# Performance work log

Hardware: AMD Instinct MI355X
Metric: run time of the kernel (lower is better)

Reference implementation:

```python
import jax, jax.numpy as jnp
import numpy as np

N = 4096
IN_F = 512
OUT_F = 256
HEADS = 4
HEAD_DIM = OUT_F // HEADS


def setup_inputs() -> dict:
    key = jax.random.key(0)
    k_feat, k_adj, k_w, k_a = jax.random.split(key, 4)
    features = jax.random.normal(k_feat, (N, IN_F), dtype=jnp.float32)
    adj_matrix = jax.random.uniform(k_adj, (N, N), dtype=jnp.float32)
    # xavier-uniform-ish init scaled small
    W = jax.random.normal(k_w, (OUT_F, IN_F), dtype=jnp.float32) * (1.0 / np.sqrt(IN_F))
    a = jax.random.normal(k_a, (HEADS, 2 * HEAD_DIM), dtype=jnp.float32) * 0.1
    bias = jnp.zeros((OUT_F,), dtype=jnp.float32)
    return {"features": features, "adj_matrix": adj_matrix, "W": W, "a": a, "bias": bias}


def reference(features, adj_matrix, W, a, bias):
    n = features.shape[0]
    h = features @ W.T                      # [N, OUT_F]
    hh = h.reshape(n, HEADS, HEAD_DIM)      # [N, H, D]
    # e[i,j,h] = leaky_relu(<h_i, a[:, :D]> + <h_j, a[:, D:]>) -- additive decomposition
    e_src = jnp.einsum('nhd,hd->nh', hh, a[:, :HEAD_DIM])   # [N, H]
    e_dst = jnp.einsum('nhd,hd->nh', hh, a[:, HEAD_DIM:])   # [N, H]
    e = e_src[:, None, :] + e_dst[None, :, :]               # [N, N, H]
    e = jnp.where(e >= 0, e, 0.2 * e)                       # leaky_relu(0.2)
    mask = adj_matrix[:, :, None] > 0.1                     # [N, N, 1]
    e = jnp.where(mask, e, -jnp.inf)
    attention = jax.nn.softmax(e, axis=1)                   # softmax over j
    attention = jnp.nan_to_num(attention, nan=0.0)          # fully-masked rows -> 0
    attention_mean = attention.mean(axis=2)                 # [N, N]
    h_out = attention_mean @ h + bias                       # [N, OUT_F]
    return h_out
```

## Files before the change

### kernel.cpp

```cpp
#include <hip/hip_runtime.h>
#include <math.h>

#define NN      4096
#define INF_    512
#define OUTF    256
#define NHEAD   4
#define HDIM    64
#define KSPLIT  8

typedef __attribute__((ext_vector_type(8))) short  short8x;
typedef __attribute__((ext_vector_type(4))) float  float4x;
typedef __attribute__((ext_vector_type(2))) float  float2x;

__device__ __forceinline__ unsigned short f2bf(float x) {
    union { float f; unsigned int u; } c; c.f = x;
    unsigned int r = (c.u + 0x7FFFu + ((c.u >> 16) & 1u)) >> 16;
    return (unsigned short)r;
}
__device__ __forceinline__ unsigned int cvtpk_bf16(float lo, float hi) {
    unsigned int r;
    asm("v_cvt_pk_bf16_f32 %0, %1, %2" : "=v"(r) : "v"(lo), "v"(hi));
    return r;
}
__device__ __forceinline__ float2x bf2up(unsigned int u) {
    union { unsigned int x; float f; } lo, hi;
    lo.x = u << 16; hi.x = u & 0xFFFF0000u;
    float2x r; r[0] = lo.f; r[1] = hi.f; return r;
}
__device__ __forceinline__ float2x max2(float2x a, float2x b) {
    float2x r; r[0] = fmaxf(a[0], b[0]); r[1] = fmaxf(a[1], b[1]); return r;
}

__global__ __launch_bounds__(256) void k_hedge(const float* __restrict__ feat,
                                               const float* __restrict__ W,
                                               const float* __restrict__ a,
                                               const float* __restrict__ bias,
                                               unsigned short* __restrict__ hT,
                                               float* __restrict__ es,
                                               unsigned short* __restrict__ Bt,
                                               unsigned short* __restrict__ Dt,
                                               float* __restrict__ out) {
    __shared__ __align__(16) unsigned short lds_f[16 * 72];
    __shared__ __align__(16) unsigned short lds_w[256 * 72];
    const int tid  = threadIdx.x;
    const int w    = tid >> 6;
    const int lane = tid & 63;
    const int lidx = lane & 15;
    const int quad = lane >> 4;
    const int i0   = blockIdx.x * 16;

    {
        float4x bv = *(const float4x*)(bias + ((tid * 4) & 255));
        float* ob = out + (size_t)i0 * OUTF;
        #pragma unroll
        for (int itr = 0; itr < 4; ++itr)
            *(float4x*)(ob + itr * 1024 + tid * 4) = bv;
    }

    const int fr = tid >> 4;
    const int fc = (tid & 15) * 4;
    const int wr = tid >> 2;
    const int wc = (tid & 3) * 16;

    float4x acc[4];
    #pragma unroll
    for (int q = 0; q < 4; ++q)
        acc[q] = (float4x){0.f, 0.f, 0.f, 0.f};

    for (int kt = 0; kt < INF_; kt += 64) {
        __syncthreads();
        {
            float4x v = *(const float4x*)&feat[(size_t)(i0 + fr) * INF_ + kt + fc];
            uint2 u;
            u.x = cvtpk_bf16(v[0], v[1]);
            u.y = cvtpk_bf16(v[2], v[3]);
            *(uint2*)&lds_f[fr * 72 + fc] = u;
        }
        #pragma unroll
        for (int p = 0; p < 4; ++p) {
            int row = p * 64 + wr;
            const float* src = &W[(size_t)row * INF_ + kt + wc];
            float4x v0 = *(const float4x*)(src);
            float4x v1 = *(const float4x*)(src + 4);
            float4x v2 = *(const float4x*)(src + 8);
            float4x v3 = *(const float4x*)(src + 12);
            union { short8x s; unsigned int u[4]; } p0, p1;
            p0.u[0] = cvtpk_bf16(v0[0], v0[1]); p0.u[1] = cvtpk_bf16(v0[2], v0[3]);
            p0.u[2] = cvtpk_bf16(v1[0], v1[1]); p0.u[3] = cvtpk_bf16(v1[2], v1[3]);
            p1.u[0] = cvtpk_bf16(v2[0], v2[1]); p1.u[1] = cvtpk_bf16(v2[2], v2[3]);
            p1.u[2] = cvtpk_bf16(v3[0], v3[1]); p1.u[3] = cvtpk_bf16(v3[2], v3[3]);
            *(short8x*)&lds_w[row * 72 + wc]     = p0.s;
            *(short8x*)&lds_w[row * 72 + wc + 8] = p1.s;
        }
        __syncthreads();
        #pragma unroll
        for (int kk = 0; kk < 2; ++kk) {
            short8x af = *(const short8x*)&lds_f[lidx * 72 + kk * 32 + quad * 8];
            short8x bw[4];
            #pragma unroll
            for (int nt = 0; nt < 4; ++nt)
                bw[nt] = *(const short8x*)&lds_w[(w * 64 + nt * 16 + lidx) * 72 + kk * 32 + quad * 8];
            #pragma unroll
            for (int nt = 0; nt < 4; ++nt)
                acc[nt] = __builtin_amdgcn_mfma_f32_16x16x32_bf16(af, bw[nt], acc[nt], 0, 0, 0);
        }
    }
    #pragma unroll
    for (int nt = 0; nt < 4; ++nt) {
        int col = w * 64 + nt * 16 + lidx;
        uint2 u;
        u.x = cvtpk_bf16(acc[nt][0], acc[nt][1]);
        u.y = cvtpk_bf16(acc[nt][2], acc[nt][3]);
        *(uint2*)&hT[(size_t)col * NN + i0 + quad * 4] = u;
    }
    float asrc[4], adst[4];
    #pragma unroll
    for (int nt = 0; nt < 4; ++nt) {
        asrc[nt] = a[w * 2 * HDIM + nt * 16 + lidx];
        adst[nt] = a[w * 2 * HDIM + HDIM + nt * 16 + lidx];
    }
    #pragma unroll
    for (int r = 0; r < 4; ++r) {
        float s = 0.f, d = 0.f;
        #pragma unroll
        for (int nt = 0; nt < 4; ++nt) {
            s += acc[nt][r] * asrc[nt];
            d += acc[nt][r] * adst[nt];
        }
        #pragma unroll
        for (int off = 1; off < 16; off <<= 1) {
            s += __shfl_xor(s, off);
            d += __shfl_xor(d, off);
        }
        if (lidx == 0) {
            int row = i0 + quad * 4 + r;
            es[row * NHEAD + w] = s;
            Bt[row * NHEAD + w] = f2bf(__expf(d));
            Dt[row * NHEAD + w] = f2bf(__expf(0.2f * d));
        }
    }
}

__global__ __launch_bounds__(256) void k_attn(const float* __restrict__ adj,
                                              const float* __restrict__ es,
                                              const unsigned short* __restrict__ Bt,
                                              const unsigned short* __restrict__ Dt,
                                              unsigned short* __restrict__ attn) {
    __shared__ float red[4][4];
    __shared__ float cfs[4];
    const int tid = threadIdx.x;
    const int wv  = tid >> 6;
    const int lane = tid & 63;
    const int i = blockIdx.x;

    const float4x esv = ((const float4x*)es)[i];
    float2x A01, A23, C01, C23;
    A01[0] = __expf(esv[0]); A01[1] = __expf(esv[1]);
    A23[0] = __expf(esv[2]); A23[1] = __expf(esv[3]);
    C01[0] = __expf(0.2f * esv[0]); C01[1] = __expf(0.2f * esv[1]);
    C23[0] = __expf(0.2f * esv[2]); C23[1] = __expf(0.2f * esv[3]);

    const float4x* arow4 = (const float4x*)(adj + (size_t)i * NN);
    const uint4* B4 = (const uint4*)Bt;
    const uint4* D4 = (const uint4*)Dt;

    float2x m01[4][4], m23[4][4];
    float2x den01 = (float2x){0.f, 0.f};
    float2x den23 = (float2x){0.f, 0.f};
    #pragma unroll
    for (int t = 0; t < 4; ++t) {
        int jv = t * 256 + tid;
        float4x av = arow4[jv];
        uint4 bu0 = B4[jv * 2], bu1 = B4[jv * 2 + 1];
        uint4 du0 = D4[jv * 2], du1 = D4[jv * 2 + 1];
        unsigned int bwv[8] = {bu0.x, bu0.y, bu0.z, bu0.w, bu1.x, bu1.y, bu1.z, bu1.w};
        unsigned int dwv[8] = {du0.x, du0.y, du0.z, du0.w, du1.x, du1.y, du1.z, du1.w};
        #pragma unroll
        for (int u = 0; u < 4; ++u) {
            float2x b01 = bf2up(bwv[u * 2]);
            float2x b23 = bf2up(bwv[u * 2 + 1]);
            float2x d01 = bf2up(dwv[u * 2]);
            float2x d23 = bf2up(dwv[u * 2 + 1]);
            float mf = (av[u] > 0.1f) ? 1.f : 0.f;
            float2x mf2; mf2[0] = mf; mf2[1] = mf;
            m01[t][u] = mf2 * max2(A01 * b01, C01 * d01);
            m23[t][u] = mf2 * max2(A23 * b23, C23 * d23);
            den01 += m01[t][u];
            den23 += m23[t][u];
        }
    }
    float dh[4] = {den01[0], den01[1], den23[0], den23[1]};
    #pragma unroll
    for (int off = 1; off < 64; off <<= 1) {
        #pragma unroll
        for (int h = 0; h < 4; ++h)
            dh[h] += __shfl_xor(dh[h], off);
    }
    if (lane == 0) {
        #pragma unroll
        for (int h = 0; h < 4; ++h) red[wv][h] = dh[h];
    }
    __syncthreads();
    if (tid < 4)
        cfs[tid] = red[0][tid] + red[1][tid] + red[2][tid] + red[3][tid];
    __syncthreads();
    float sc[4];
    #pragma unroll
    for (int h = 0; h < 4; ++h) {
        float den = cfs[h];
        sc[h] = den > 0.f ? 0.25f / den : 0.f;
    }

    unsigned short* orow = attn + (size_t)i * NN;
    #pragma unroll
    for (int t = 0; t < 4; ++t) {
        int jv = t * 256 + tid;
        float pv[4];
        #pragma unroll
        for (int u = 0; u < 4; ++u) {
            pv[u] = sc[0] * m01[t][u][0] + sc[1] * m01[t][u][1]
                  + sc[2] * m23[t][u][0] + sc[3] * m23[t][u][1];
        }
        uint2 o;
        o.x = cvtpk_bf16(pv[0], pv[1]);
        o.y = cvtpk_bf16(pv[2], pv[3]);
        *(uint2*)&orow[jv * 4] = o;
    }
}

__global__ __launch_bounds__(256) void k_out_gemm(const unsigned short* __restrict__ attn,
                                                  const unsigned short* __restrict__ hT,
                                                  float* __restrict__ out) {
    __shared__ __align__(16) unsigned short lds_a[32 * 72];
    __shared__ __align__(16) unsigned short lds_h[256 * 72];
    const int tid  = threadIdx.x;
    const int w    = tid >> 6;
    const int lane = tid & 63;
    const int lidx = lane & 15;
    const int quad = lane >> 4;
    const int i0    = blockIdx.x * 32;
    const int kbase = blockIdx.y * (NN / KSPLIT);
    const int sr   = tid >> 3;
    const int sc   = (tid & 7) * 8;

    float4x acc[2][4];
    #pragma unroll
    for (int p = 0; p < 2; ++p)
        #pragma unroll
        for (int q = 0; q < 4; ++q)
            acc[p][q] = (float4x){0.f, 0.f, 0.f, 0.f};

    short8x pa;
    short8x ph[8];
    pa = *(const short8x*)&attn[(size_t)(i0 + sr) * NN + kbase + sc];
    #pragma unroll
    for (int p = 0; p < 8; ++p)
        ph[p] = *(const short8x*)&hT[(size_t)(p * 32 + sr) * NN + kbase + sc];

    const int KSTEPS = (NN / KSPLIT) / 64;
    for (int ks = 0; ks < KSTEPS; ++ks) {
        __syncthreads();
        *(short8x*)&lds_a[sr * 72 + sc] = pa;
        #pragma unroll
        for (int p = 0; p < 8; ++p)
            *(short8x*)&lds_h[(p * 32 + sr) * 72 + sc] = ph[p];
        __syncthreads();
        if (ks + 1 < KSTEPS) {
            const int ko = kbase + (ks + 1) * 64;
            pa = *(const short8x*)&attn[(size_t)(i0 + sr) * NN + ko + sc];
            #pragma unroll
            for (int p = 0; p < 8; ++p)
                ph[p] = *(const short8x*)&hT[(size_t)(p * 32 + sr) * NN + ko + sc];
        }
        #pragma unroll
        for (int kk = 0; kk < 2; ++kk) {
            short8x af[2], bfr[4];
            #pragma unroll
            for (int it = 0; it < 2; ++it)
                af[it]  = *(const short8x*)&lds_a[(it * 16 + lidx) * 72 + kk * 32 + quad * 8];
            #pragma unroll
            for (int nt = 0; nt < 4; ++nt)
                bfr[nt] = *(const short8x*)&lds_h[(w * 64 + nt * 16 + lidx) * 72 + kk * 32 + quad * 8];
            #pragma unroll
            for (int it = 0; it < 2; ++it)
                #pragma unroll
                for (int nt = 0; nt < 4; ++nt)
                    acc[it][nt] = __builtin_amdgcn_mfma_f32_16x16x32_bf16(
                        af[it], bfr[nt], acc[it][nt], 0, 0, 0);
        }
    }
    #pragma unroll
    for (int it = 0; it < 2; ++it)
        #pragma unroll
        for (int nt = 0; nt < 4; ++nt)
            #pragma unroll
            for (int rr = 0; rr < 4; ++rr) {
                int row = i0 + it * 16 + quad * 4 + rr;
                int col = w * 64 + nt * 16 + lidx;
                unsafeAtomicAdd(&out[(size_t)row * OUTF + col], acc[it][nt][rr]);
            }
}

extern "C" void kernel_launch(void* const* d_in, const int* in_sizes, int n_in,
                              void* d_out, int out_size, void* d_ws, size_t ws_size,
                              hipStream_t stream) {
    const float* feat = (const float*)d_in[0];
    const float* adj  = (const float*)d_in[1];
    const float* W    = (const float*)d_in[2];
    const float* a    = (const float*)d_in[3];
    const float* bias = (const float*)d_in[4];
    float* out = (float*)d_out;

    char* ws = (char*)d_ws;
    float*          es    = (float*)(ws + 0);
    unsigned short* Btb   = (unsigned short*)(ws + (64u << 10));
    unsigned short* Dtb   = (unsigned short*)(ws + (96u << 10));
    unsigned short* hT    = (unsigned short*)(ws + (256u << 10));
    unsigned short* attn  = (unsigned short*)(ws + (2560u << 10));

    k_hedge    <<<256,               256, 0, stream>>>(feat, W, a, bias, hT, es, Btb, Dtb, out);
    k_attn     <<<NN,                256, 0, stream>>>(adj, es, Btb, Dtb, attn);
    k_out_gemm <<<dim3(128, KSPLIT), 256, 0, stream>>>(attn, hT, out);
}
```

Baseline: 170.9 us.

## Precompute adjacency bitmask in extra blocks of the projection kernel

```diff
diff --git a/kernel.cpp b/kernel.cpp
--- a/kernel.cpp
+++ b/kernel.cpp
@@ -35,14 +35,36 @@
                                                const float* __restrict__ W,
                                                const float* __restrict__ a,
                                                const float* __restrict__ bias,
+                                               const float* __restrict__ adj,
                                                unsigned short* __restrict__ hT,
                                                float* __restrict__ es,
                                                unsigned short* __restrict__ Bt,
                                                unsigned short* __restrict__ Dt,
+                                               unsigned short* __restrict__ mask,
                                                float* __restrict__ out) {
     __shared__ __align__(16) unsigned short lds_f[16 * 72];
     __shared__ __align__(16) unsigned short lds_w[256 * 72];
     const int tid  = threadIdx.x;
+
+    if (blockIdx.x >= 256) {
+        const int mb = blockIdx.x - 256;
+        #pragma unroll
+        for (int r = 0; r < 2; ++r) {
+            const int row = mb * 2 + r;
+            const float4x* arow4 = (const float4x*)(adj + (size_t)row * NN);
+            unsigned int bits = 0;
+            #pragma unroll
+            for (int t = 0; t < 4; ++t) {
+                float4x av = arow4[t * 256 + tid];
+                #pragma unroll
+                for (int e = 0; e < 4; ++e)
+                    bits |= (av[e] > 0.1f ? 1u : 0u) << (t * 4 + e);
+            }
+            mask[(size_t)row * 256 + tid] = (unsigned short)bits;
+        }
+        return;
+    }
+
     const int w    = tid >> 6;
     const int lane = tid & 63;
     const int lidx = lane & 15;
@@ -141,7 +163,7 @@
     }
 }
 
-__global__ __launch_bounds__(256) void k_attn(const float* __restrict__ adj,
+__global__ __launch_bounds__(256) void k_attn(const unsigned short* __restrict__ mask,
                                               const float* __restrict__ es,
                                               const unsigned short* __restrict__ Bt,
                                               const unsigned short* __restrict__ Dt,
@@ -160,7 +182,7 @@
     C01[0] = __expf(0.2f * esv[0]); C01[1] = __expf(0.2f * esv[1]);
     C23[0] = __expf(0.2f * esv[2]); C23[1] = __expf(0.2f * esv[3]);
 
-    const float4x* arow4 = (const float4x*)(adj + (size_t)i * NN);
+    const unsigned int mbits = mask[(size_t)i * 256 + tid];
     const uint4* B4 = (const uint4*)Bt;
     const uint4* D4 = (const uint4*)Dt;
 
@@ -170,7 +192,6 @@
     #pragma unroll
     for (int t = 0; t < 4; ++t) {
         int jv = t * 256 + tid;
-        float4x av = arow4[jv];
         uint4 bu0 = B4[jv * 2], bu1 = B4[jv * 2 + 1];
         uint4 du0 = D4[jv * 2], du1 = D4[jv * 2 + 1];
         unsigned int bwv[8] = {bu0.x, bu0.y, bu0.z, bu0.w, bu1.x, bu1.y, bu1.z, bu1.w};
@@ -181,7 +202,7 @@
             float2x b23 = bf2up(bwv[u * 2 + 1]);
             float2x d01 = bf2up(dwv[u * 2]);
             float2x d23 = bf2up(dwv[u * 2 + 1]);
-            float mf = (av[u] > 0.1f) ? 1.f : 0.f;
+            float mf = (mbits & (1u << (t * 4 + u))) ? 1.f : 0.f;
             float2x mf2; mf2[0] = mf; mf2[1] = mf;
             m01[t][u] = mf2 * max2(A01 * b01, C01 * d01);
             m23[t][u] = mf2 * max2(A23 * b23, C23 * d23);
@@ -315,10 +336,11 @@
     float*          es    = (float*)(ws + 0);
     unsigned short* Btb   = (unsigned short*)(ws + (64u << 10));
     unsigned short* Dtb   = (unsigned short*)(ws + (96u << 10));
-    unsigned short* hT    = (unsigned short*)(ws + (256u << 10));
-    unsigned short* attn  = (unsigned short*)(ws + (2560u << 10));
-
-    k_hedge    <<<256,               256, 0, stream>>>(feat, W, a, bias, hT, es, Btb, Dtb, out);
-    k_attn     <<<NN,                256, 0, stream>>>(adj, es, Btb, Dtb, attn);
+    unsigned short* mask  = (unsigned short*)(ws + (128u << 10));
+    unsigned short* hT    = (unsigned short*)(ws + (2560u << 10));
+    unsigned short* attn  = (unsigned short*)(ws + (5120u << 10));
+
+    k_hedge    <<<2304,              256, 0, stream>>>(feat, W, a, bias, adj, hT, es, Btb, Dtb, mask, out);
+    k_attn     <<<NN,                256, 0, stream>>>(mask, es, Btb, Dtb, attn);
     k_out_gemm <<<dim3(128, KSPLIT), 256, 0, stream>>>(attn, hT, out);
 }
```

New measurement: 169.8 us. Within noise of the previous version (-0.6%).
